# Kernel optimization log

Measured on AMD Instinct MI355X. Metric: run time of the kernel, lower is better.

Reference implementation:

```python
import jax, jax.numpy as jnp
import numpy as np
import math

N, E, D, R, L = 20000, 640000, 128, 16, 3
R_MAX = math.sqrt(2.0)
CENTERS = jnp.linspace(0.0, R_MAX, R)          # GaussianRBF centers on [0, sqrt(2)]
GAMMA = 1.0 / (2.0 * (R_MAX / (R - 1)) ** 2)   # 1/(2*sigma^2), sigma = center spacing


def _mlp(x, w1, b1, w2, b2):
    # mlp([din, d_h, dout]): Linear -> SiLU -> Linear (dropout=0.0)
    return jax.nn.silu(x @ w1 + b1) @ w2 + b2


def _ln(x, g, b):
    mu = jnp.mean(x, axis=-1, keepdims=True)
    v = jnp.var(x, axis=-1, keepdims=True)
    return (x - mu) * jax.lax.rsqrt(v + 1e-5) * g + b


def _time_emb(t):
    # SinusoidalEmbedding(dim=D)
    half = D // 2
    freqs = jnp.exp(-math.log(10000.0) * jnp.arange(half, dtype=jnp.float32) / (half - 1))
    a = t * freqs
    return jnp.concatenate([jnp.sin(a), jnp.cos(a)])


def setup_inputs():
    key = jax.random.key(0)
    ks = jax.random.split(key, 16)
    s = 0.05
    p = {}
    p["x_t"] = jax.random.normal(ks[0], (N, 3), dtype=jnp.float32)
    p["edge_index"] = jax.random.randint(ks[1], (2, E), 0, N)
    p["t"] = 25
    p["time_w1"] = jax.random.normal(ks[2], (D, D)) * s
    p["time_b1"] = jnp.zeros((D,))
    p["time_w2"] = jax.random.normal(ks[3], (D, D)) * s
    p["time_b2"] = jnp.zeros((D,))
    p["nodein_w1"] = jax.random.normal(ks[4], (3 + D, D)) * s
    p["nodein_b1"] = jnp.zeros((D,))
    p["nodein_w2"] = jax.random.normal(ks[5], (D, D)) * s
    p["nodein_b2"] = jnp.zeros((D,))
    p["phim_w1"] = jax.random.normal(ks[6], (L, 2 * D + R, D)) * s
    p["phim_b1"] = jnp.zeros((L, D))
    p["phim_w2"] = jax.random.normal(ks[7], (L, D, D)) * s
    p["phim_b2"] = jnp.zeros((L, D))
    p["phih_w1"] = jax.random.normal(ks[8], (L, 2 * D, D)) * s
    p["phih_b1"] = jnp.zeros((L, D))
    p["phih_w2"] = jax.random.normal(ks[9], (L, D, D)) * s
    p["phih_b2"] = jnp.zeros((L, D))
    p["ln_g"] = jnp.ones((L, D))
    p["ln_b"] = jnp.zeros((L, D))
    p["out_w1"] = jax.random.normal(ks[10], (D, D)) * s
    p["out_b1"] = jnp.zeros((D,))
    p["out_w2"] = jax.random.normal(ks[11], (D, 3)) * s
    p["out_b2"] = jnp.zeros((3,))
    return p


def reference(x_t, edge_index, t,
              time_w1, time_b1, time_w2, time_b2,
              nodein_w1, nodein_b1, nodein_w2, nodein_b2,
              phim_w1, phim_b1, phim_w2, phim_b2,
              phih_w1, phih_b1, phih_w2, phih_b2,
              ln_g, ln_b,
              out_w1, out_b1, out_w2, out_b2):
    # GraphDenoiser.forward: one denoiser call of the diffusion sampling loop.
    n = x_t.shape[0]
    src, dst = edge_index[0], edge_index[1]

    te = _mlp(_time_emb(jnp.asarray(t, jnp.float32)), time_w1, time_b1, time_w2, time_b2)
    h = _mlp(jnp.concatenate([x_t, jnp.broadcast_to(te, (n, D))], axis=-1),
             nodein_w1, nodein_b1, nodein_w2, nodein_b2)

    # edge geometry is fixed across layers (depends only on x_t)
    dx = x_t[src, :2] - x_t[dst, :2]                     # [E, 2]
    r = jnp.sqrt(jnp.sum(dx * dx, axis=-1) + 1e-8)       # [E]
    rbf = jnp.exp(-GAMMA * (r[:, None] - CENTERS) ** 2)  # [E, R]

    for i in range(L):  # WeightedInvariantMPNNLayer x L (edge_weight == 1)
        m_in = jnp.concatenate([h[src], h[dst], rbf], axis=-1)      # [E, 2D+R]
        m = _mlp(m_in, phim_w1[i], phim_b1[i], phim_w2[i], phim_b2[i])
        agg = jax.ops.segment_sum(m, dst, num_segments=n)           # scatter_sum
        h_up = _mlp(jnp.concatenate([h, agg], axis=-1),
                    phih_w1[i], phih_b1[i], phih_w2[i], phih_b2[i])
        h = _ln(h + h_up, ln_g[i], ln_b[i])

    return _mlp(h, out_w1, out_b1, out_w2, out_b2)  # predicted eps, [N, 3]
```

## Files before the change

kernel.cpp:

```cpp
#include <hip/hip_runtime.h>

typedef unsigned short u16;
typedef unsigned int u32;

#define NNODES 20000
#define NEDGES 640000
#define RBF_GAMMA 56.25f
#define SQRT2 1.4142135623730951f
#define PITCH 132
#define BPITCH 136

typedef __bf16 bf16x8 __attribute__((ext_vector_type(8)));
typedef __bf16 bf16x2 __attribute__((ext_vector_type(2)));
typedef float f32x4 __attribute__((ext_vector_type(4)));

__device__ __forceinline__ float b2f(u16 u) {
    union { float f; u32 i; } x; x.i = ((u32)u) << 16; return x.f;
}
__device__ __forceinline__ float hi2f(u32 w) {
    union { float f; u32 i; } x; x.i = w & 0xffff0000u; return x.f;
}
__device__ __forceinline__ float lo2f(u32 w) {
    union { float f; u32 i; } x; x.i = w << 16; return x.f;
}
__device__ __forceinline__ u16 f2b(float f) {
    union { float f; u32 i; } x; x.f = f;
    u32 r = (x.i + 0x7fffu + ((x.i >> 16) & 1u)) >> 16;
    return (u16)r;
}
__device__ __forceinline__ u32 pack2(float a, float b) {
#if __has_builtin(__builtin_amdgcn_cvt_pk_bf16_f32)
    union { bf16x2 v; u32 u; } x;
    x.v = __builtin_amdgcn_cvt_pk_bf16_f32(a, b);
    return x.u;
#else
    return (u32)f2b(a) | ((u32)f2b(b) << 16);
#endif
}
__device__ __forceinline__ float silu(float v) {
    return v * __builtin_amdgcn_rcpf(1.0f + __expf(-v));
}
__device__ __forceinline__ void fma4(float4 w, float4 s, float& acc) {
    acc = fmaf(w.x, s.x, acc);
    acc = fmaf(w.y, s.y, acc);
    acc = fmaf(w.z, s.z, acc);
    acc = fmaf(w.w, s.w, acc);
}

__global__ __launch_bounds__(256) void k_hist(const int* __restrict__ ei, int* __restrict__ hist) {
    int e = blockIdx.x * 256 + threadIdx.x;
    atomicAdd(&hist[ei[NEDGES + e]], 1);
}

__global__ __launch_bounds__(1024) void k_scan(const int* __restrict__ hist,
                                               int* __restrict__ row_ptr,
                                               int* __restrict__ cursor) {
    __shared__ int psum[1024];
    int t = threadIdx.x;
    int base = t * 20;
    int s = 0;
    if (base < NNODES)
        for (int i = 0; i < 20; ++i) s += hist[base + i];
    psum[t] = s;
    __syncthreads();
    for (int off = 1; off < 1024; off <<= 1) {
        int v = (t >= off) ? psum[t - off] : 0;
        __syncthreads();
        psum[t] += v;
        __syncthreads();
    }
    int excl = psum[t] - s;
    if (base < NNODES) {
        int run = excl;
        for (int i = 0; i < 20; ++i) {
            row_ptr[base + i] = run;
            cursor[base + i] = run;
            run += hist[base + i];
        }
    }
    if (t == 1023) row_ptr[NNODES] = psum[1023];
}

__global__ __launch_bounds__(256) void k_scatter(const int* __restrict__ ei, int* __restrict__ cursor,
                                                 int* __restrict__ ssrc, int* __restrict__ sdst) {
    int e = blockIdx.x * 256 + threadIdx.x;
    int d = ei[NEDGES + e];
    int pos = atomicAdd(&cursor[d], 1);
    ssrc[pos] = ei[e];
    sdst[pos] = d;
}

__global__ __launch_bounds__(256) void k_prep_wr(const float* __restrict__ pmw1,
                                                 const float* __restrict__ pmb1,
                                                 u16* __restrict__ Wr) {
    int id = blockIdx.x * 256 + threadIdx.x;
    if (id >= 1536) return;
    int l = id / 512; int r = id - l * 512;
    int nt = r >> 6, lane = r & 63;
    int col = nt * 16 + (lane & 15);
    alignas(16) u16 tmp[8];
    #pragma unroll
    for (int jj = 0; jj < 8; ++jj) {
        int kk = (lane >> 4) * 8 + jj;
        float v = 0.f;
        if (kk < 16) v = pmw1[l * 34816 + (256 + kk) * 128 + col];
        else if (kk == 16) v = pmb1[l * 128 + col];
        tmp[jj] = f2b(v);
    }
    *(uint4*)(Wr + (size_t)id * 8) = *(const uint4*)tmp;
}

struct BfM { const float* s[16]; };
__global__ __launch_bounds__(256) void k_prep_bf(BfM bf, u16* __restrict__ dst) {
    int id = blockIdx.x * 256 + threadIdx.x;
    if (id >= 32768) return;
    int mat = id >> 11;
    bool lomode = (mat >= 13);
    int r = id & 2047;
    int kc = r >> 9;
    int r2 = r & 511;
    int nt = r2 >> 6, lane = r2 & 63;
    int col = nt * 16 + (lane & 15);
    int kb = kc * 32 + (lane >> 4) * 8;
    const float* src = bf.s[mat];
    alignas(16) u16 tmp[8];
    #pragma unroll
    for (int jj = 0; jj < 8; ++jj) {
        float v = src[(kb + jj) * 128 + col];
        u16 h = f2b(v);
        tmp[jj] = lomode ? f2b(v - b2f(h)) : h;
    }
    *(uint4*)(dst + (size_t)id * 8) = *(const uint4*)tmp;
}

__global__ __launch_bounds__(256) void k_prep_mbf(const float* __restrict__ Mp, u16* __restrict__ dst) {
    int id = blockIdx.x * 256 + threadIdx.x;
    if (id >= 12288) return;
    int mat = id >> 11;
    int l = mat >> 1, lomode = mat & 1;
    int r = id & 2047;
    int kc = r >> 9;
    int r2 = r & 511;
    int nt = r2 >> 6, lane = r2 & 63;
    int col = nt * 16 + (lane & 15);
    int kb = kc * 32 + (lane >> 4) * 8;
    const float* src = Mp + (size_t)l * 16384;
    alignas(16) u16 tmp[8];
    #pragma unroll
    for (int jj = 0; jj < 8; ++jj) {
        int k = kb + jj;
        float v = src[(k >> 2) * 512 + col * 4 + (k & 3)];
        u16 h = f2b(v);
        tmp[jj] = lomode ? f2b(v - b2f(h)) : h;
    }
    *(uint4*)(dst + (size_t)id * 8) = *(const uint4*)tmp;
}

struct PackM { const float* s[4]; float* d[4]; int K[4]; };
__global__ __launch_bounds__(256) void k_pack(PackM pm) {
    int m = blockIdx.y;
    int idx = blockIdx.x * 256 + threadIdx.x;
    if (idx >= pm.K[m] * 128) return;
    int k = idx >> 7, j = idx & 127;
    pm.d[m][(k >> 2) * 512 + j * 4 + (k & 3)] = pm.s[m][idx];
}

__global__ __launch_bounds__(256) void k_prep_m(const float* __restrict__ pmw2,
        const float* __restrict__ pmb2, const float* __restrict__ V1p,
        float* __restrict__ Mp, float* __restrict__ bvv) {
    const int l = blockIdx.y, bx = blockIdx.x;
    const float* V1 = V1p + (size_t)l * 32768;
    const int tid = threadIdx.x;
    const int w = tid >> 6, lane = tid & 63;
    const int cg = lane & 15, ng = lane >> 4;
    const int jc0 = w * 32 + cg * 2, jc1 = jc0 + 1;
    __shared__ alignas(16) float W2L[16][PITCH];
    __shared__ float b2L[128];
    if (bx < 8) {
        const float4* src = (const float4*)(pmw2 + (size_t)l * 16384 + bx * 16 * 128);
        for (int q = tid; q < 512; q += 256) {
            int row = q >> 5, part = q & 31;
            *(float4*)&W2L[row][part * 4] = src[q];
        }
        __syncthreads();
        int r0 = ng * 4;
        float acc[4][2];
        #pragma unroll
        for (int n = 0; n < 4; ++n) { acc[n][0] = 0.f; acc[n][1] = 0.f; }
        for (int mm = 0; mm < 32; ++mm) {
            float4 wa = *(const float4*)(V1 + (32 + mm) * 512 + jc0 * 4);
            float4 wb = *(const float4*)(V1 + (32 + mm) * 512 + jc1 * 4);
            #pragma unroll
            for (int n = 0; n < 4; ++n) {
                float4 s4 = *(const float4*)&W2L[r0 + n][mm * 4];
                fma4(wa, s4, acc[n][0]);
                fma4(wb, s4, acc[n][1]);
            }
        }
        #pragma unroll
        for (int n = 0; n < 4; ++n) {
            int kg = bx * 16 + r0 + n;
            Mp[(size_t)l * 16384 + (kg >> 2) * 512 + jc0 * 4 + (kg & 3)] = acc[n][0];
            Mp[(size_t)l * 16384 + (kg >> 2) * 512 + jc1 * 4 + (kg & 3)] = acc[n][1];
        }
    } else {
        if (tid < 128) b2L[tid] = pmb2[l * 128 + tid];
        __syncthreads();
        if (ng == 0) {
            float a0 = 0.f, a1 = 0.f;
            for (int mm = 0; mm < 32; ++mm) {
                float4 wa = *(const float4*)(V1 + (32 + mm) * 512 + jc0 * 4);
                float4 wb = *(const float4*)(V1 + (32 + mm) * 512 + jc1 * 4);
                float4 s4 = *(const float4*)&b2L[mm * 4];
                fma4(wa, s4, a0);
                fma4(wb, s4, a1);
            }
            bvv[l * 128 + jc0] = a0;
            bvv[l * 128 + jc1] = a1;
        }
    }
}

__global__ __launch_bounds__(128) void k_time(const int* __restrict__ tptr,
        const float* __restrict__ tw1, const float* __restrict__ tb1,
        const float* __restrict__ tw2, const float* __restrict__ tb2,
        const float* __restrict__ nw1, const float* __restrict__ nb1,
        float* __restrict__ base1) {
    __shared__ float emb[128], hid[128], te[128];
    int j = threadIdx.x;
    int raw = tptr[0];
    float tv;
    if (raw >= 0 && raw < (1 << 24)) tv = (float)raw;
    else tv = __int_as_float(raw);
    float fr = expf(-9.210340371976184f * (float)(j & 63) / 63.0f);
    float a = tv * fr;
    emb[j] = (j < 64) ? sinf(a) : cosf(a);
    __syncthreads();
    float acc = tb1[j];
    for (int k = 0; k < 128; ++k) acc += emb[k] * tw1[k * 128 + j];
    hid[j] = silu(acc);
    __syncthreads();
    acc = tb2[j];
    for (int k = 0; k < 128; ++k) acc += hid[k] * tw2[k * 128 + j];
    te[j] = acc;
    __syncthreads();
    acc = nb1[j];
    for (int k = 0; k < 128; ++k) acc += te[k] * nw1[(3 + k) * 128 + j];
    base1[j] = acc;
}

__global__ __launch_bounds__(256) void k_h0(const float* __restrict__ x, const float* __restrict__ base1,
        const float* __restrict__ nw1, const float* __restrict__ nw2p, const float* __restrict__ nb2,
        const u16* __restrict__ Yw,
        float* __restrict__ hf, u16* __restrict__ Ysrc, u16* __restrict__ Ydst) {
    const int tid = threadIdx.x;
    const int w = tid >> 6, lane = tid & 63;
    const int cg = lane & 15, ng = lane >> 4;
    const int jc0 = w * 32 + cg * 2, jc1 = jc0 + 1;
    const int n0 = ng * 4;
    const int base = blockIdx.x * 16;
    __shared__ alignas(16) float xl[16][4];
    __shared__ alignas(16) float hid[16][PITCH];
    __shared__ alignas(16) u16 hb16[16 * BPITCH];
    if (tid < 48) { int n = tid / 3, cc = tid - n * 3; xl[n][cc] = x[(size_t)(base + n) * 3 + cc]; }
    __syncthreads();
    {
        float w0a = nw1[jc0], w0b = nw1[jc1];
        float w1a = nw1[128 + jc0], w1b = nw1[128 + jc1];
        float w2a = nw1[256 + jc0], w2b = nw1[256 + jc1];
        float ba = base1[jc0], bb = base1[jc1];
        #pragma unroll
        for (int n = 0; n < 4; ++n) {
            int row = n0 + n;
            float x0 = xl[row][0], x1 = xl[row][1], x2 = xl[row][2];
            float2 v;
            v.x = silu(ba + x0 * w0a + x1 * w1a + x2 * w2a);
            v.y = silu(bb + x0 * w0b + x1 * w1b + x2 * w2b);
            *(float2*)&hid[row][jc0] = v;
        }
    }
    __syncthreads();
    float acc[4][2];
    {
        float ba = nb2[jc0], bb = nb2[jc1];
        #pragma unroll
        for (int n = 0; n < 4; ++n) { acc[n][0] = ba; acc[n][1] = bb; }
        for (int kk = 0; kk < 32; ++kk) {
            float4 wa = *(const float4*)(nw2p + kk * 512 + jc0 * 4);
            float4 wb = *(const float4*)(nw2p + kk * 512 + jc1 * 4);
            #pragma unroll
            for (int n = 0; n < 4; ++n) {
                float4 s4 = *(const float4*)&hid[n0 + n][kk * 4];
                fma4(wa, s4, acc[n][0]);
                fma4(wb, s4, acc[n][1]);
            }
        }
    }
    __syncthreads();
    #pragma unroll
    for (int n = 0; n < 4; ++n) {
        int row = n0 + n;
        *(float2*)&hf[(size_t)(base + row) * 128 + jc0] = make_float2(acc[n][0], acc[n][1]);
        *(u32*)&hb16[row * BPITCH + jc0] = pack2(acc[n][0], acc[n][1]);
    }
    __syncthreads();
    {
        const int mat = w >> 1, half = w & 1;
        const int lrow = lane & 15, quad = lane >> 4;
        bf16x8 a[4];
        #pragma unroll
        for (int kc = 0; kc < 4; ++kc)
            a[kc] = *(const bf16x8*)(hb16 + lrow * BPITCH + kc * 32 + quad * 8);
        u16* dst = mat ? Ydst : Ysrc;
        #pragma unroll
        for (int t = 0; t < 4; ++t) {
            int nt = half * 4 + t;
            f32x4 a4 = {0.f, 0.f, 0.f, 0.f};
            #pragma unroll
            for (int kc = 0; kc < 4; ++kc) {
                bf16x8 b = *(const bf16x8*)(Yw + (size_t)(((mat * 4 + kc) * 8 + nt) * 512 + lane * 8));
                a4 = __builtin_amdgcn_mfma_f32_16x16x32_bf16(a[kc], b, a4, 0, 0, 0);
            }
            #pragma unroll
            for (int r = 0; r < 4; ++r)
                dst[(size_t)(base + quad * 4 + r) * 128 + nt * 16 + lrow] = f2b(a4[r]);
        }
    }
}

__global__ __launch_bounds__(512, 8) void k_edge(
        const u16* __restrict__ Ysrc, const u16* __restrict__ Ydst,
        const float* __restrict__ x,
        const int* __restrict__ ssrc, const int* __restrict__ sdst,
        const u16* __restrict__ Wr,
        float* __restrict__ s_glob) {
    __shared__ alignas(16) u16 sst[128 * 72];
    __shared__ alignas(16) u16 ys[64 * 128];
    __shared__ float rv[64];
    __shared__ int s_d[65];
    __shared__ int s_s[64];
    const int tid = threadIdx.x;
    const int e0 = blockIdx.x * 64;
    if (tid < 64) {
        int s = ssrc[e0 + tid], d = sdst[e0 + tid];
        s_s[tid] = s; s_d[tid] = d;
        float ddx = x[s * 3] - x[d * 3];
        float ddy = x[s * 3 + 1] - x[d * 3 + 1];
        rv[tid] = sqrtf(ddx * ddx + ddy * ddy + 1e-8f);
    } else if (tid == 64) {
        s_d[64] = -1;
    }
    __syncthreads();
    #pragma unroll
    for (int i = 0; i < 2; ++i) {
        int cch = tid + i * 512;
        int e = cch >> 4, part = cch & 15;
        *(uint4*)(ys + e * 128 + part * 8) = *(const uint4*)(Ysrc + (size_t)s_s[e] * 128 + part * 8);
    }
    const int w = tid >> 6, lane = tid & 63;
    const int m = w & 3, nh = w >> 2;
    const int lrow = lane & 15, quad = lane >> 4;
    float r = rv[m * 16 + lrow];
    union { bf16x8 v; u16 u[8]; } af;
    #pragma unroll
    for (int j = 0; j < 8; ++j) {
        int kk = quad * 8 + j;
        float v;
        if (kk < 16) {
            float dd = r - SQRT2 * (float)kk / 15.0f;
            v = __expf(-RBF_GAMMA * dd * dd);
        } else v = (kk == 16) ? 1.0f : 0.0f;
        af.u[j] = f2b(v);
    }
    {
        const u16* Bp = Wr + lane * 8;
        #pragma unroll
        for (int t = 0; t < 4; ++t) {
            int nt = nh * 4 + t;
            f32x4 a4 = {0.f, 0.f, 0.f, 0.f};
            bf16x8 b = *(const bf16x8*)(Bp + nt * 512);
            a4 = __builtin_amdgcn_mfma_f32_16x16x32_bf16(af.v, b, a4, 0, 0, 0);
            int col = nt * 16 + lrow;
            u32 lo = pack2(a4[0], a4[1]);
            u32 hi = pack2(a4[2], a4[3]);
            *(uint2*)(sst + col * 72 + m * 16 + quad * 4) = make_uint2(lo, hi);
        }
    }
    __syncthreads();
    {
        const int col = tid & 127, q = tid >> 7;
        const int r0 = q * 16;
        float a = 0.f;
        int cd = s_d[r0];
        float yd = b2f(Ydst[(size_t)cd * 128 + col]);
        #pragma unroll
        for (int h = 0; h < 2; ++h) {
            uint4 c0 = *(const uint4*)(sst + col * 72 + r0 + h * 8);
            float sv8[8];
            sv8[0] = lo2f(c0.x); sv8[1] = hi2f(c0.x);
            sv8[2] = lo2f(c0.y); sv8[3] = hi2f(c0.y);
            sv8[4] = lo2f(c0.z); sv8[5] = hi2f(c0.z);
            sv8[6] = lo2f(c0.w); sv8[7] = hi2f(c0.w);
            #pragma unroll
            for (int i = 0; i < 8; ++i) {
                int rr = r0 + h * 8 + i;
                int nd = s_d[rr + 1];
                float v = sv8[i] + b2f(ys[rr * 128 + col]) + yd;
                a += silu(v);
                bool last = (h == 1 && i == 7);
                if (last || nd != cd) {
                    atomicAdd(&s_glob[(size_t)cd * 128 + col], a);
                    a = 0.f;
                    if (!last && nd != cd)
                        yd = b2f(Ydst[(size_t)nd * 128 + col]);
                }
                cd = nd;
            }
        }
    }
}

__global__ __launch_bounds__(256) void k_node(float* __restrict__ s_glob, const int* __restrict__ row_ptr,
        float* __restrict__ hf,
        const u16* __restrict__ V1h, const u16* __restrict__ V1l,
        const u16* __restrict__ Mh, const u16* __restrict__ Ml,
        const u16* __restrict__ V2bf,
        const float* __restrict__ bv, const float* __restrict__ c1, const float* __restrict__ c2,
        const float* __restrict__ lng, const float* __restrict__ lnb,
        const u16* __restrict__ Yw,
        u16* __restrict__ Ysrc, u16* __restrict__ Ydst) {
    const int tid = threadIdx.x;
    const int w = tid >> 6, lane = tid & 63;
    const int cg = lane & 15, ng = lane >> 4;
    const int jc0 = w * 32 + cg * 2, jc1 = jc0 + 1;
    const int n0 = ng * 4;
    const int base = blockIdx.x * 16;
    const int lrow = lane & 15, quad = lane >> 4;
    __shared__ alignas(16) float hv[16][PITCH];
    __shared__ alignas(16) float xs[16][PITCH];
    __shared__ alignas(16) u16 hvh[16 * BPITCH], hvl[16 * BPITCH];
    __shared__ alignas(16) u16 svh[16 * BPITCH], svl[16 * BPITCH];
    __shared__ alignas(16) u16 ybf[16 * BPITCH];
    __shared__ float mv[16][2];
    __shared__ int rp[17];

    if (tid < 17) rp[tid] = row_ptr[base + tid];
    {
        const float4* sg4 = (const float4*)(s_glob + (size_t)base * 128);
        float4* sg4w = (float4*)(s_glob + (size_t)base * 128);
        const float4* hg4 = (const float4*)(hf + (size_t)base * 128);
        for (int q = tid; q < 512; q += 256) {
            int row = q >> 5, part = q & 31;
            float4 s = sg4[q];
            float4 h = hg4[q];
            sg4w[q] = make_float4(0.f, 0.f, 0.f, 0.f);
            *(float4*)&hv[row][part * 4] = h;
            u32 hw0 = pack2(h.x, h.y), hw1 = pack2(h.z, h.w);
            *(uint2*)&hvh[row * BPITCH + part * 4] = make_uint2(hw0, hw1);
            u32 hl0 = pack2(h.x - lo2f(hw0), h.y - hi2f(hw0));
            u32 hl1 = pack2(h.z - lo2f(hw1), h.w - hi2f(hw1));
            *(uint2*)&hvl[row * BPITCH + part * 4] = make_uint2(hl0, hl1);
            u32 sw0 = pack2(s.x, s.y), sw1 = pack2(s.z, s.w);
            *(uint2*)&svh[row * BPITCH + part * 4] = make_uint2(sw0, sw1);
            u32 sl0 = pack2(s.x - lo2f(sw0), s.y - hi2f(sw0));
            u32 sl1 = pack2(s.z - lo2f(sw1), s.w - hi2f(sw1));
            *(uint2*)&svl[row * BPITCH + part * 4] = make_uint2(sl0, sl1);
        }
    }
    __syncthreads();

    {
        bf16x8 ahh[4], ahl[4], ash[4], asl[4];
        #pragma unroll
        for (int kc = 0; kc < 4; ++kc) {
            ahh[kc] = *(const bf16x8*)(hvh + lrow * BPITCH + kc * 32 + quad * 8);
            ahl[kc] = *(const bf16x8*)(hvl + lrow * BPITCH + kc * 32 + quad * 8);
            ash[kc] = *(const bf16x8*)(svh + lrow * BPITCH + kc * 32 + quad * 8);
            asl[kc] = *(const bf16x8*)(svl + lrow * BPITCH + kc * 32 + quad * 8);
        }
        float dg[4];
        #pragma unroll
        for (int r = 0; r < 4; ++r)
            dg[r] = (float)(rp[quad * 4 + r + 1] - rp[quad * 4 + r]);
        #pragma unroll
        for (int t = 0; t < 2; ++t) {
            int nt = w * 2 + t;
            f32x4 a4 = {0.f, 0.f, 0.f, 0.f};
            #pragma unroll
            for (int kc = 0; kc < 4; ++kc) {
                size_t o = (size_t)((kc * 8 + nt) * 512 + lane * 8);
                bf16x8 bh = *(const bf16x8*)(V1h + o);
                bf16x8 bl = *(const bf16x8*)(V1l + o);
                a4 = __builtin_amdgcn_mfma_f32_16x16x32_bf16(ahh[kc], bh, a4, 0, 0, 0);
                a4 = __builtin_amdgcn_mfma_f32_16x16x32_bf16(ahl[kc], bh, a4, 0, 0, 0);
                a4 = __builtin_amdgcn_mfma_f32_16x16x32_bf16(ahh[kc], bl, a4, 0, 0, 0);
                bf16x8 mh = *(const bf16x8*)(Mh + o);
                bf16x8 ml = *(const bf16x8*)(Ml + o);
                a4 = __builtin_amdgcn_mfma_f32_16x16x32_bf16(ash[kc], mh, a4, 0, 0, 0);
                a4 = __builtin_amdgcn_mfma_f32_16x16x32_bf16(asl[kc], mh, a4, 0, 0, 0);
                a4 = __builtin_amdgcn_mfma_f32_16x16x32_bf16(ash[kc], ml, a4, 0, 0, 0);
            }
            int colC = nt * 16 + lrow;
            float bvC = bv[colC], c1C = c1[colC];
            #pragma unroll
            for (int r = 0; r < 4; ++r) {
                float u = a4[r] + dg[r] * bvC + c1C;
                ybf[(quad * 4 + r) * BPITCH + colC] = f2b(silu(u));
            }
        }
    }
    __syncthreads();
    {
        bf16x8 a[4];
        #pragma unroll
        for (int kc = 0; kc < 4; ++kc)
            a[kc] = *(const bf16x8*)(ybf + lrow * BPITCH + kc * 32 + quad * 8);
        #pragma unroll
        for (int t = 0; t < 2; ++t) {
            int nt = w * 2 + t;
            f32x4 a4 = {0.f, 0.f, 0.f, 0.f};
            #pragma unroll
            for (int kc = 0; kc < 4; ++kc) {
                bf16x8 b = *(const bf16x8*)(V2bf + (size_t)((kc * 8 + nt) * 512 + lane * 8));
                a4 = __builtin_amdgcn_mfma_f32_16x16x32_bf16(a[kc], b, a4, 0, 0, 0);
            }
            int colC = nt * 16 + lrow;
            float c2v = c2[colC];
            #pragma unroll
            for (int r = 0; r < 4; ++r) {
                int R = quad * 4 + r;
                xs[R][colC] = a4[r] + c2v + hv[R][colC];
            }
        }
    }
    __syncthreads();
    {
        int row = tid >> 4, part = tid & 15;
        float4 a = *(const float4*)&xs[row][part * 8];
        float4 b = *(const float4*)&xs[row][part * 8 + 4];
        float s1 = a.x + a.y + a.z + a.w + b.x + b.y + b.z + b.w;
        float s2 = a.x * a.x + a.y * a.y + a.z * a.z + a.w * a.w
                 + b.x * b.x + b.y * b.y + b.z * b.z + b.w * b.w;
        #pragma unroll
        for (int mq = 1; mq < 16; mq <<= 1) {
            s1 += __shfl_xor(s1, mq, 64);
            s2 += __shfl_xor(s2, mq, 64);
        }
        if (part == 0) { mv[row][0] = s1; mv[row][1] = s2; }
    }
    __syncthreads();
    {
        float ga = lng[jc0], gb = lng[jc1];
        float bba = lnb[jc0], bbb = lnb[jc1];
        #pragma unroll
        for (int n = 0; n < 4; ++n) {
            int row = n0 + n;
            float mu = mv[row][0] * (1.0f / 128.0f);
            float var = mv[row][1] * (1.0f / 128.0f) - mu * mu;
            float rs = rsqrtf(var + 1e-5f);
            float y0 = (xs[row][jc0] - mu) * rs * ga + bba;
            float y1 = (xs[row][jc1] - mu) * rs * gb + bbb;
            *(float2*)&hf[(size_t)(base + row) * 128 + jc0] = make_float2(y0, y1);
            *(u32*)&ybf[row * BPITCH + jc0] = pack2(y0, y1);
        }
    }
    if (Yw != nullptr) {
        __syncthreads();
        const int mat = w >> 1, half = w & 1;
        bf16x8 a[4];
        #pragma unroll
        for (int kc = 0; kc < 4; ++kc)
            a[kc] = *(const bf16x8*)(ybf + lrow * BPITCH + kc * 32 + quad * 8);
        u16* dst = mat ? Ydst : Ysrc;
        #pragma unroll
        for (int t = 0; t < 4; ++t) {
            int nt = half * 4 + t;
            f32x4 a4 = {0.f, 0.f, 0.f, 0.f};
            #pragma unroll
            for (int kc = 0; kc < 4; ++kc) {
                bf16x8 b = *(const bf16x8*)(Yw + (size_t)(((mat * 4 + kc) * 8 + nt) * 512 + lane * 8));
                a4 = __builtin_amdgcn_mfma_f32_16x16x32_bf16(a[kc], b, a4, 0, 0, 0);
            }
            #pragma unroll
            for (int r = 0; r < 4; ++r)
                dst[(size_t)(base + quad * 4 + r) * 128 + nt * 16 + lrow] = f2b(a4[r]);
        }
    }
}

__global__ __launch_bounds__(256) void k_out(const float* __restrict__ hf, const u16* __restrict__ ow1bf,
        const float* __restrict__ ob1, const float* __restrict__ ow2, const float* __restrict__ ob2,
        float* __restrict__ out) {
    const int tid = threadIdx.x;
    const int w = tid >> 6, lane = tid & 63;
    const int lrow = lane & 15, quad = lane >> 4;
    const int base = blockIdx.x * 16;
    __shared__ alignas(16) u16 hb16[16 * BPITCH];
    __shared__ float hid[16][PITCH];
    for (int q = tid; q < 512; q += 256) {
        int row = q >> 5, part = q & 31;
        float4 v = ((const float4*)(hf + (size_t)base * 128))[q];
        *(uint2*)&hb16[row * BPITCH + part * 4] = make_uint2(pack2(v.x, v.y), pack2(v.z, v.w));
    }
    __syncthreads();
    {
        bf16x8 a[4];
        #pragma unroll
        for (int kc = 0; kc < 4; ++kc)
            a[kc] = *(const bf16x8*)(hb16 + lrow * BPITCH + kc * 32 + quad * 8);
        #pragma unroll
        for (int t = 0; t < 2; ++t) {
            int nt = w * 2 + t;
            f32x4 a4 = {0.f, 0.f, 0.f, 0.f};
            #pragma unroll
            for (int kc = 0; kc < 4; ++kc) {
                bf16x8 b = *(const bf16x8*)(ow1bf + (size_t)((kc * 8 + nt) * 512 + lane * 8));
                a4 = __builtin_amdgcn_mfma_f32_16x16x32_bf16(a[kc], b, a4, 0, 0, 0);
            }
            int colC = nt * 16 + lrow;
            float b1v = ob1[colC];
            #pragma unroll
            for (int r = 0; r < 4; ++r)
                hid[quad * 4 + r][colC] = silu(a4[r] + b1v);
        }
    }
    __syncthreads();
    if (tid < 48) {
        int n = tid / 3, cc = tid - n * 3;
        float o = ob2[cc];
        for (int k = 0; k < 128; ++k) o += hid[n][k] * ow2[k * 3 + cc];
        out[(size_t)(base + n) * 3 + cc] = o;
    }
}

extern "C" void kernel_launch(void* const* d_in, const int* in_sizes, int n_in,
                              void* d_out, int out_size, void* d_ws, size_t ws_size,
                              hipStream_t stream) {
    const float* x    = (const float*)d_in[0];
    const int* ei     = (const int*)d_in[1];
    const int* tptr   = (const int*)d_in[2];
    const float* tw1  = (const float*)d_in[3];
    const float* tb1  = (const float*)d_in[4];
    const float* tw2  = (const float*)d_in[5];
    const float* tb2  = (const float*)d_in[6];
    const float* nw1  = (const float*)d_in[7];
    const float* nb1  = (const float*)d_in[8];
    const float* nw2  = (const float*)d_in[9];
    const float* nb2  = (const float*)d_in[10];
    const float* pmw1 = (const float*)d_in[11];
    const float* pmb1 = (const float*)d_in[12];
    const float* pmw2 = (const float*)d_in[13];
    const float* pmb2 = (const float*)d_in[14];
    const float* phw1 = (const float*)d_in[15];
    const float* phb1 = (const float*)d_in[16];
    const float* phw2 = (const float*)d_in[17];
    const float* phb2 = (const float*)d_in[18];
    const float* lng  = (const float*)d_in[19];
    const float* lnb  = (const float*)d_in[20];
    const float* ow1  = (const float*)d_in[21];
    const float* ob1  = (const float*)d_in[22];
    const float* ow2  = (const float*)d_in[23];
    const float* ob2  = (const float*)d_in[24];
    float* out = (float*)d_out;

    char* wsp = (char*)d_ws;
    size_t off = 0;
    auto alloc = [&](size_t bytes) -> void* {
        void* p = wsp + off;
        off += (bytes + 255) & ~(size_t)255;
        return p;
    };
    int* hist    = (int*)alloc((size_t)NNODES * 4);
    int* cursor  = (int*)alloc((size_t)NNODES * 4);
    int* row_ptr = (int*)alloc((size_t)(NNODES + 1) * 4);
    int* ssrc    = (int*)alloc((size_t)NEDGES * 4);
    int* sdst    = (int*)alloc((size_t)NEDGES * 4);
    u16* Wr      = (u16*)alloc((size_t)3 * 8 * 64 * 8 * 2);
    u16* BF      = (u16*)alloc((size_t)16 * 16384 * 2);
    u16* Mf      = (u16*)alloc((size_t)6 * 16384 * 2);
    float* base1 = (float*)alloc(128 * 4);
    float* V1p   = (float*)alloc((size_t)3 * 256 * 128 * 4);
    float* nw2p  = (float*)alloc((size_t)128 * 128 * 4);
    float* Mp    = (float*)alloc((size_t)3 * 128 * 128 * 4);
    float* bvv   = (float*)alloc((size_t)3 * 128 * 4);
    float* hf    = (float*)alloc((size_t)NNODES * 128 * 4);
    u16* Ysrc    = (u16*)alloc((size_t)NNODES * 128 * 2);
    u16* Ydst    = (u16*)alloc((size_t)NNODES * 128 * 2);
    float* s_glob= (float*)alloc((size_t)NNODES * 128 * 4);

    (void)hipMemsetAsync(hist, 0, (size_t)NNODES * 4, stream);
    k_hist<<<NEDGES / 256, 256, 0, stream>>>(ei, hist);
    k_scan<<<1, 1024, 0, stream>>>(hist, row_ptr, cursor);
    k_scatter<<<NEDGES / 256, 256, 0, stream>>>(ei, cursor, ssrc, sdst);
    k_prep_wr<<<6, 256, 0, stream>>>(pmw1, pmb1, Wr);

    BfM bf;
    for (int l = 0; l < 3; ++l) {
        bf.s[l * 2 + 0] = pmw1 + (size_t)l * 34816;
        bf.s[l * 2 + 1] = pmw1 + (size_t)l * 34816 + 16384;
        bf.s[6 + l] = phw2 + (size_t)l * 16384;
        bf.s[10 + l] = phw1 + (size_t)l * 32768;
        bf.s[13 + l] = phw1 + (size_t)l * 32768;
    }
    bf.s[9] = ow1;
    k_prep_bf<<<128, 256, 0, stream>>>(bf, BF);

    PackM pm;
    for (int l = 0; l < 3; ++l) {
        pm.s[l] = phw1 + (size_t)l * 32768; pm.d[l] = V1p + (size_t)l * 32768; pm.K[l] = 256;
    }
    pm.s[3] = nw2; pm.d[3] = nw2p; pm.K[3] = 128;
    k_pack<<<dim3(128, 4), 256, 0, stream>>>(pm);
    k_prep_m<<<dim3(9, 3), 256, 0, stream>>>(pmw2, pmb2, V1p, Mp, bvv);
    k_prep_mbf<<<48, 256, 0, stream>>>(Mp, Mf);

    k_time<<<1, 128, 0, stream>>>(tptr, tw1, tb1, tw2, tb2, nw1, nb1, base1);
    k_h0<<<1250, 256, 0, stream>>>(x, base1, nw1, nw2p, nb2, BF, hf, Ysrc, Ydst);

    (void)hipMemsetAsync(s_glob, 0, (size_t)NNODES * 128 * 4, stream);
    for (int l = 0; l < 3; ++l) {
        k_edge<<<NEDGES / 64, 512, 0, stream>>>(Ysrc, Ydst, x, ssrc, sdst,
                Wr + (size_t)l * 4096, s_glob);
        const u16* YwN = (l < 2) ? (BF + (size_t)(l + 1) * 32768) : nullptr;
        k_node<<<1250, 256, 0, stream>>>(s_glob, row_ptr, hf,
                BF + (size_t)(10 + l) * 16384, BF + (size_t)(13 + l) * 16384,
                Mf + (size_t)(l * 2) * 16384, Mf + (size_t)(l * 2 + 1) * 16384,
                BF + (size_t)(6 + l) * 16384,
                bvv + l * 128, phb1 + l * 128, phb2 + l * 128, lng + l * 128, lnb + l * 128,
                YwN, Ysrc, Ydst);
    }
    k_out<<<1250, 256, 0, stream>>>(hf, BF + (size_t)9 * 16384, ob1, ow2, ob2, out);
}
```

Measured before the change: 519.2 us.

## Fuse output MLP into last node kernel and move h0 second GEMM to MFMA

```diff
diff --git a/kernel.cpp b/kernel.cpp
--- a/kernel.cpp
+++ b/kernel.cpp
@@ -110,12 +110,12 @@
     *(uint4*)(Wr + (size_t)id * 8) = *(const uint4*)tmp;
 }
 
-struct BfM { const float* s[16]; };
+struct BfM { const float* s[18]; };
 __global__ __launch_bounds__(256) void k_prep_bf(BfM bf, u16* __restrict__ dst) {
     int id = blockIdx.x * 256 + threadIdx.x;
-    if (id >= 32768) return;
+    if (id >= 36864) return;
     int mat = id >> 11;
-    bool lomode = (mat >= 13);
+    bool lomode = (mat >= 13 && mat != 16);
     int r = id & 2047;
     int kc = r >> 9;
     int r2 = r & 511;
@@ -156,7 +156,7 @@
     *(uint4*)(dst + (size_t)id * 8) = *(const uint4*)tmp;
 }
 
-struct PackM { const float* s[4]; float* d[4]; int K[4]; };
+struct PackM { const float* s[3]; float* d[3]; int K[3]; };
 __global__ __launch_bounds__(256) void k_pack(PackM pm) {
     int m = blockIdx.y;
     int idx = blockIdx.x * 256 + threadIdx.x;
@@ -250,8 +250,8 @@
 }
 
 __global__ __launch_bounds__(256) void k_h0(const float* __restrict__ x, const float* __restrict__ base1,
-        const float* __restrict__ nw1, const float* __restrict__ nw2p, const float* __restrict__ nb2,
-        const u16* __restrict__ Yw,
+        const float* __restrict__ nw1, const u16* __restrict__ nw2h, const u16* __restrict__ nw2l,
+        const float* __restrict__ nb2, const u16* __restrict__ Yw,
         float* __restrict__ hf, u16* __restrict__ Ysrc, u16* __restrict__ Ydst) {
     const int tid = threadIdx.x;
     const int w = tid >> 6, lane = tid & 63;
@@ -259,8 +259,9 @@
     const int jc0 = w * 32 + cg * 2, jc1 = jc0 + 1;
     const int n0 = ng * 4;
     const int base = blockIdx.x * 16;
+    const int lrow = lane & 15, quad = lane >> 4;
     __shared__ alignas(16) float xl[16][4];
-    __shared__ alignas(16) float hid[16][PITCH];
+    __shared__ alignas(16) u16 hih[16 * BPITCH], hil[16 * BPITCH];
     __shared__ alignas(16) u16 hb16[16 * BPITCH];
     if (tid < 48) { int n = tid / 3, cc = tid - n * 3; xl[n][cc] = x[(size_t)(base + n) * 3 + cc]; }
     __syncthreads();
@@ -273,40 +274,48 @@
         for (int n = 0; n < 4; ++n) {
             int row = n0 + n;
             float x0 = xl[row][0], x1 = xl[row][1], x2 = xl[row][2];
-            float2 v;
-            v.x = silu(ba + x0 * w0a + x1 * w1a + x2 * w2a);
-            v.y = silu(bb + x0 * w0b + x1 * w1b + x2 * w2b);
-            *(float2*)&hid[row][jc0] = v;
-        }
-    }
-    __syncthreads();
-    float acc[4][2];
-    {
-        float ba = nb2[jc0], bb = nb2[jc1];
-        #pragma unroll
-        for (int n = 0; n < 4; ++n) { acc[n][0] = ba; acc[n][1] = bb; }
-        for (int kk = 0; kk < 32; ++kk) {
-            float4 wa = *(const float4*)(nw2p + kk * 512 + jc0 * 4);
-            float4 wb = *(const float4*)(nw2p + kk * 512 + jc1 * 4);
-            #pragma unroll
-            for (int n = 0; n < 4; ++n) {
-                float4 s4 = *(const float4*)&hid[n0 + n][kk * 4];
-                fma4(wa, s4, acc[n][0]);
-                fma4(wb, s4, acc[n][1]);
-            }
-        }
-    }
-    __syncthreads();
-    #pragma unroll
-    for (int n = 0; n < 4; ++n) {
-        int row = n0 + n;
-        *(float2*)&hf[(size_t)(base + row) * 128 + jc0] = make_float2(acc[n][0], acc[n][1]);
-        *(u32*)&hb16[row * BPITCH + jc0] = pack2(acc[n][0], acc[n][1]);
+            float va = silu(ba + x0 * w0a + x1 * w1a + x2 * w2a);
+            float vb = silu(bb + x0 * w0b + x1 * w1b + x2 * w2b);
+            u32 hw = pack2(va, vb);
+            *(u32*)&hih[row * BPITCH + jc0] = hw;
+            *(u32*)&hil[row * BPITCH + jc0] = pack2(va - lo2f(hw), vb - hi2f(hw));
+        }
+    }
+    __syncthreads();
+    {
+        bf16x8 ah[4], al[4];
+        #pragma unroll
+        for (int kc = 0; kc < 4; ++kc) {
+            ah[kc] = *(const bf16x8*)(hih + lrow * BPITCH + kc * 32 + quad * 8);
+            al[kc] = *(const bf16x8*)(hil + lrow * BPITCH + kc * 32 + quad * 8);
+        }
+        #pragma unroll
+        for (int t = 0; t < 2; ++t) {
+            int nt = w * 2 + t;
+            f32x4 a4 = {0.f, 0.f, 0.f, 0.f};
+            #pragma unroll
+            for (int kc = 0; kc < 4; ++kc) {
+                size_t o = (size_t)((kc * 8 + nt) * 512 + lane * 8);
+                bf16x8 bh = *(const bf16x8*)(nw2h + o);
+                bf16x8 bl = *(const bf16x8*)(nw2l + o);
+                a4 = __builtin_amdgcn_mfma_f32_16x16x32_bf16(ah[kc], bh, a4, 0, 0, 0);
+                a4 = __builtin_amdgcn_mfma_f32_16x16x32_bf16(al[kc], bh, a4, 0, 0, 0);
+                a4 = __builtin_amdgcn_mfma_f32_16x16x32_bf16(ah[kc], bl, a4, 0, 0, 0);
+            }
+            int colC = nt * 16 + lrow;
+            float bC = nb2[colC];
+            #pragma unroll
+            for (int r = 0; r < 4; ++r) {
+                int R = quad * 4 + r;
+                float v = a4[r] + bC;
+                hf[(size_t)(base + R) * 128 + colC] = v;
+                hb16[R * BPITCH + colC] = f2b(v);
+            }
+        }
     }
     __syncthreads();
     {
         const int mat = w >> 1, half = w & 1;
-        const int lrow = lane & 15, quad = lane >> 4;
         bf16x8 a[4];
         #pragma unroll
         for (int kc = 0; kc < 4; ++kc)
@@ -428,7 +437,10 @@
         const float* __restrict__ bv, const float* __restrict__ c1, const float* __restrict__ c2,
         const float* __restrict__ lng, const float* __restrict__ lnb,
         const u16* __restrict__ Yw,
-        u16* __restrict__ Ysrc, u16* __restrict__ Ydst) {
+        u16* __restrict__ Ysrc, u16* __restrict__ Ydst,
+        const u16* __restrict__ ow1bf, const float* __restrict__ ob1,
+        const float* __restrict__ ow2, const float* __restrict__ ob2,
+        float* __restrict__ out) {
     const int tid = threadIdx.x;
     const int w = tid >> 6, lane = tid & 63;
     const int cg = lane & 15, ng = lane >> 4;
@@ -453,7 +465,7 @@
             int row = q >> 5, part = q & 31;
             float4 s = sg4[q];
             float4 h = hg4[q];
-            sg4w[q] = make_float4(0.f, 0.f, 0.f, 0.f);
+            if (Yw != nullptr) sg4w[q] = make_float4(0.f, 0.f, 0.f, 0.f);
             *(float4*)&hv[row][part * 4] = h;
             u32 hw0 = pack2(h.x, h.y), hw1 = pack2(h.z, h.w);
             *(uint2*)&hvh[row * BPITCH + part * 4] = make_uint2(hw0, hw1);
@@ -560,7 +572,8 @@
             float rs = rsqrtf(var + 1e-5f);
             float y0 = (xs[row][jc0] - mu) * rs * ga + bba;
             float y1 = (xs[row][jc1] - mu) * rs * gb + bbb;
-            *(float2*)&hf[(size_t)(base + row) * 128 + jc0] = make_float2(y0, y1);
+            if (Yw != nullptr)
+                *(float2*)&hf[(size_t)(base + row) * 128 + jc0] = make_float2(y0, y1);
             *(u32*)&ybf[row * BPITCH + jc0] = pack2(y0, y1);
         }
     }
@@ -585,51 +598,54 @@
             for (int r = 0; r < 4; ++r)
                 dst[(size_t)(base + quad * 4 + r) * 128 + nt * 16 + lrow] = f2b(a4[r]);
         }
-    }
-}
-
-__global__ __launch_bounds__(256) void k_out(const float* __restrict__ hf, const u16* __restrict__ ow1bf,
-        const float* __restrict__ ob1, const float* __restrict__ ow2, const float* __restrict__ ob2,
-        float* __restrict__ out) {
-    const int tid = threadIdx.x;
-    const int w = tid >> 6, lane = tid & 63;
-    const int lrow = lane & 15, quad = lane >> 4;
-    const int base = blockIdx.x * 16;
-    __shared__ alignas(16) u16 hb16[16 * BPITCH];
-    __shared__ float hid[16][PITCH];
-    for (int q = tid; q < 512; q += 256) {
-        int row = q >> 5, part = q & 31;
-        float4 v = ((const float4*)(hf + (size_t)base * 128))[q];
-        *(uint2*)&hb16[row * BPITCH + part * 4] = make_uint2(pack2(v.x, v.y), pack2(v.z, v.w));
-    }
-    __syncthreads();
-    {
-        bf16x8 a[4];
-        #pragma unroll
-        for (int kc = 0; kc < 4; ++kc)
-            a[kc] = *(const bf16x8*)(hb16 + lrow * BPITCH + kc * 32 + quad * 8);
-        #pragma unroll
-        for (int t = 0; t < 2; ++t) {
-            int nt = w * 2 + t;
-            f32x4 a4 = {0.f, 0.f, 0.f, 0.f};
-            #pragma unroll
-            for (int kc = 0; kc < 4; ++kc) {
-                bf16x8 b = *(const bf16x8*)(ow1bf + (size_t)((kc * 8 + nt) * 512 + lane * 8));
-                a4 = __builtin_amdgcn_mfma_f32_16x16x32_bf16(a[kc], b, a4, 0, 0, 0);
-            }
-            int colC = nt * 16 + lrow;
-            float b1v = ob1[colC];
-            #pragma unroll
-            for (int r = 0; r < 4; ++r)
-                hid[quad * 4 + r][colC] = silu(a4[r] + b1v);
-        }
-    }
-    __syncthreads();
-    if (tid < 48) {
-        int n = tid / 3, cc = tid - n * 3;
-        float o = ob2[cc];
-        for (int k = 0; k < 128; ++k) o += hid[n][k] * ow2[k * 3 + cc];
-        out[(size_t)(base + n) * 3 + cc] = o;
+    } else {
+        __syncthreads();
+        {
+            bf16x8 a[4];
+            #pragma unroll
+            for (int kc = 0; kc < 4; ++kc)
+                a[kc] = *(const bf16x8*)(ybf + lrow * BPITCH + kc * 32 + quad * 8);
+            #pragma unroll
+            for (int t = 0; t < 2; ++t) {
+                int nt = w * 2 + t;
+                f32x4 a4 = {0.f, 0.f, 0.f, 0.f};
+                #pragma unroll
+                for (int kc = 0; kc < 4; ++kc) {
+                    bf16x8 b = *(const bf16x8*)(ow1bf + (size_t)((kc * 8 + nt) * 512 + lane * 8));
+                    a4 = __builtin_amdgcn_mfma_f32_16x16x32_bf16(a[kc], b, a4, 0, 0, 0);
+                }
+                int colC = nt * 16 + lrow;
+                float b1v = ob1[colC];
+                #pragma unroll
+                for (int r = 0; r < 4; ++r)
+                    hv[quad * 4 + r][colC] = silu(a4[r] + b1v);
+            }
+        }
+        __syncthreads();
+        {
+            int row = tid >> 4, s = tid & 15;
+            float p0 = 0.f, p1 = 0.f, p2 = 0.f;
+            #pragma unroll
+            for (int kk2 = 0; kk2 < 8; ++kk2) {
+                int k = s * 8 + kk2;
+                float h2 = hv[row][k];
+                p0 = fmaf(h2, ow2[k * 3 + 0], p0);
+                p1 = fmaf(h2, ow2[k * 3 + 1], p1);
+                p2 = fmaf(h2, ow2[k * 3 + 2], p2);
+            }
+            #pragma unroll
+            for (int mq = 1; mq < 16; mq <<= 1) {
+                p0 += __shfl_xor(p0, mq, 64);
+                p1 += __shfl_xor(p1, mq, 64);
+                p2 += __shfl_xor(p2, mq, 64);
+            }
+            if (s == 0) {
+                float* o = out + (size_t)(base + row) * 3;
+                o[0] = p0 + ob2[0];
+                o[1] = p1 + ob2[1];
+                o[2] = p2 + ob2[2];
+            }
+        }
     }
 }
 
@@ -676,11 +692,10 @@
     int* ssrc    = (int*)alloc((size_t)NEDGES * 4);
     int* sdst    = (int*)alloc((size_t)NEDGES * 4);
     u16* Wr      = (u16*)alloc((size_t)3 * 8 * 64 * 8 * 2);
-    u16* BF      = (u16*)alloc((size_t)16 * 16384 * 2);
+    u16* BF      = (u16*)alloc((size_t)18 * 16384 * 2);
     u16* Mf      = (u16*)alloc((size_t)6 * 16384 * 2);
     float* base1 = (float*)alloc(128 * 4);
     float* V1p   = (float*)alloc((size_t)3 * 256 * 128 * 4);
-    float* nw2p  = (float*)alloc((size_t)128 * 128 * 4);
     float* Mp    = (float*)alloc((size_t)3 * 128 * 128 * 4);
     float* bvv   = (float*)alloc((size_t)3 * 128 * 4);
     float* hf    = (float*)alloc((size_t)NNODES * 128 * 4);
@@ -703,19 +718,21 @@
         bf.s[13 + l] = phw1 + (size_t)l * 32768;
     }
     bf.s[9] = ow1;
-    k_prep_bf<<<128, 256, 0, stream>>>(bf, BF);
+    bf.s[16] = nw2;
+    bf.s[17] = nw2;
+    k_prep_bf<<<144, 256, 0, stream>>>(bf, BF);
 
     PackM pm;
     for (int l = 0; l < 3; ++l) {
         pm.s[l] = phw1 + (size_t)l * 32768; pm.d[l] = V1p + (size_t)l * 32768; pm.K[l] = 256;
     }
-    pm.s[3] = nw2; pm.d[3] = nw2p; pm.K[3] = 128;
-    k_pack<<<dim3(128, 4), 256, 0, stream>>>(pm);
+    k_pack<<<dim3(128, 3), 256, 0, stream>>>(pm);
     k_prep_m<<<dim3(9, 3), 256, 0, stream>>>(pmw2, pmb2, V1p, Mp, bvv);
     k_prep_mbf<<<48, 256, 0, stream>>>(Mp, Mf);
 
     k_time<<<1, 128, 0, stream>>>(tptr, tw1, tb1, tw2, tb2, nw1, nb1, base1);
-    k_h0<<<1250, 256, 0, stream>>>(x, base1, nw1, nw2p, nb2, BF, hf, Ysrc, Ydst);
+    k_h0<<<1250, 256, 0, stream>>>(x, base1, nw1,
+            BF + (size_t)16 * 16384, BF + (size_t)17 * 16384, nb2, BF, hf, Ysrc, Ydst);
 
     (void)hipMemsetAsync(s_glob, 0, (size_t)NNODES * 128 * 4, stream);
     for (int l = 0; l < 3; ++l) {
@@ -727,7 +744,7 @@
                 Mf + (size_t)(l * 2) * 16384, Mf + (size_t)(l * 2 + 1) * 16384,
                 BF + (size_t)(6 + l) * 16384,
                 bvv + l * 128, phb1 + l * 128, phb2 + l * 128, lng + l * 128, lnb + l * 128,
-                YwN, Ysrc, Ydst);
-    }
-    k_out<<<1250, 256, 0, stream>>>(hf, BF + (size_t)9 * 16384, ob1, ow2, ob2, out);
-}
+                YwN, Ysrc, Ydst,
+                BF + (size_t)9 * 16384, ob1, ow2, ob2, out);
+    }
+}
```

After: 505.3 us. -2.7%, faster.
